# Kernel optimization log

Hardware: AMD Instinct MI355X
Metric: run time of the kernel (lower is better)

## Reference

```python
import jax, jax.numpy as jnp
import numpy as np

N = 50000       # nodes
E = 1600000     # edges (before self-loops)
H = 4           # heads
C = 32          # channels per head
G = 64          # graphs in batch
NEG_SLOPE = 0.2


def gat_conv(x, src, dst, W, att_src, att_dst, bias):
    # x: [N, Fin]; W: [Fin, H*C]; att_*: [H, C]; bias: [H*C]
    h = (x @ W).reshape(N, H, C)                       # [N, H, C]
    a_src = jnp.einsum('nhc,hc->nh', h, att_src)       # [N, H]
    a_dst = jnp.einsum('nhc,hc->nh', h, att_dst)       # [N, H]
    e = a_src[src] + a_dst[dst]                        # [E', H]
    e = jax.nn.leaky_relu(e, NEG_SLOPE)
    # softmax over incoming edges of each destination node
    m = jax.ops.segment_max(e, dst, num_segments=N)    # [N, H]
    ex = jnp.exp(e - m[dst])
    denom = jax.ops.segment_sum(ex, dst, num_segments=N)  # [N, H]
    alpha = ex / (denom[dst] + 1e-16)                  # [E', H]
    msg = h[src] * alpha[:, :, None]                   # [E', H, C]
    out = jax.ops.segment_sum(msg, dst, num_segments=N)  # [N, H, C]
    return out.reshape(N, H * C) + bias


def setup_inputs() -> dict:
    key = jax.random.key(0)
    ks = jax.random.split(key, 12)
    x = jax.random.normal(ks[0], (N, 128), dtype=jnp.float32)
    edge_index = jax.random.randint(ks[1], (2, E), 0, N, dtype=jnp.int64)
    batch = jnp.sort(jax.random.randint(ks[2], (N,), 0, G, dtype=jnp.int64))
    s = 0.05
    return {
        'x': x,
        'edge_index': edge_index,
        'batch': batch,
        'W1': jax.random.normal(ks[3], (128, H * C), dtype=jnp.float32) * s,
        'att_src1': jax.random.normal(ks[4], (H, C), dtype=jnp.float32) * s,
        'att_dst1': jax.random.normal(ks[5], (H, C), dtype=jnp.float32) * s,
        'b1': jnp.zeros((H * C,), dtype=jnp.float32),
        'W2': jax.random.normal(ks[6], (H * C, H * C), dtype=jnp.float32) * s,
        'att_src2': jax.random.normal(ks[7], (H, C), dtype=jnp.float32) * s,
        'att_dst2': jax.random.normal(ks[8], (H, C), dtype=jnp.float32) * s,
        'b2': jnp.zeros((H * C,), dtype=jnp.float32),
        'fc_W': jax.random.normal(ks[9], (H * C, 8), dtype=jnp.float32) * s,
        'fc_b': jnp.zeros((8,), dtype=jnp.float32),
    }


def reference(x, edge_index, batch, W1, att_src1, att_dst1, b1,
              W2, att_src2, att_dst2, b2, fc_W, fc_b):
    # add self loops (PyG GATConv default)
    ar = jnp.arange(N, dtype=edge_index.dtype)
    src = jnp.concatenate([edge_index[0], ar])
    dst = jnp.concatenate([edge_index[1], ar])
    h = gat_conv(x, src, dst, W1, att_src1, att_dst1, b1)
    h = jax.nn.elu(h)
    h = gat_conv(h, src, dst, W2, att_src2, att_dst2, b2)
    # global mean pool over graphs
    sums = jax.ops.segment_sum(h, batch, num_segments=G)          # [G, HC]
    cnt = jax.ops.segment_sum(jnp.ones((N,), h.dtype), batch, num_segments=G)
    pooled = sums / jnp.maximum(cnt, 1.0)[:, None]
    logits = pooled @ fc_W + fc_b                                  # [G, 8]
    return jax.nn.log_softmax(logits, axis=1)
```

## Files before the change

### kernel.cpp

```cpp
#include <hip/hip_runtime.h>
#include <math.h>

#define HC 128
#define GG 64
#define NEG 0.2f
#define TILE 8192
#define BW 128
#define SLOT 8192
#define LDA 136
#define GBS 32

typedef __attribute__((ext_vector_type(8))) short short8;
typedef __attribute__((ext_vector_type(4))) float floatx4;
typedef __attribute__((ext_vector_type(2))) float floatx2;

static __device__ __forceinline__ float leaky(float x) { return x > 0.f ? x : NEG * x; }

static __device__ __forceinline__ unsigned short f2bf(float f) {
    unsigned u = __float_as_uint(f);
    u += 0x7FFF + ((u >> 16) & 1);
    return (unsigned short)(u >> 16);
}

#if __has_builtin(__builtin_amdgcn_cvt_pk_f32_fp8) && __has_builtin(__builtin_amdgcn_cvt_pk_fp8_f32)
template <bool HI>
static __device__ __forceinline__ floatx2 fp8pair(unsigned int w) {
    return __builtin_amdgcn_cvt_pk_f32_fp8((int)w, HI);
}
static __device__ __forceinline__ unsigned int f32x2_fp8(float a, float b) {
    return ((unsigned int)__builtin_amdgcn_cvt_pk_fp8_f32(a, b, 0, false)) & 0xFFFFu;
}
#else
static __device__ __forceinline__ float fp8one(unsigned v) {
    unsigned e = (v >> 3) & 15u, m = v & 7u;
    float mag = e ? __uint_as_float(((e + 120u) << 23) | (m << 20))
                  : (float)m * 0.001953125f;
    return (v & 0x80u) ? -mag : mag;
}
template <bool HI>
static __device__ __forceinline__ floatx2 fp8pair(unsigned int w) {
    unsigned h = HI ? (w >> 16) : w;
    floatx2 r; r.x = fp8one(h & 0xFFu); r.y = fp8one((h >> 8) & 0xFFu);
    return r;
}
static __device__ __forceinline__ unsigned fp8enc(float f) {
    unsigned u = __float_as_uint(f);
    unsigned s = (u >> 24) & 0x80u;
    float a = fabsf(f);
    if (a >= 448.f) return s | 0x7Eu;
    if (a < 0.015625f) {
        unsigned m = (unsigned)(int)rintf(a * 512.f);
        return s | m;
    }
    u = __float_as_uint(a);
    u += 0xFFFFFu + ((u >> 20) & 1u);
    unsigned e8 = (u >> 23) - 120u;
    if (e8 >= 16u) return s | 0x7Eu;
    return s | (e8 << 3) | ((u >> 20) & 7u);
}
static __device__ __forceinline__ unsigned int f32x2_fp8(float a, float b) {
    return fp8enc(a) | (fp8enc(b) << 8);
}
#endif

static __device__ __forceinline__ void acc16(floatx2* acc, float w, const uint4& d) {
    floatx2 w2 = {w, w};
    acc[0] += w2 * fp8pair<false>(d.x);
    acc[1] += w2 * fp8pair<true>(d.x);
    acc[2] += w2 * fp8pair<false>(d.y);
    acc[3] += w2 * fp8pair<true>(d.y);
    acc[4] += w2 * fp8pair<false>(d.z);
    acc[5] += w2 * fp8pair<true>(d.z);
    acc[6] += w2 * fp8pair<false>(d.w);
    acc[7] += w2 * fp8pair<true>(d.w);
}

__global__ __launch_bounds__(256) void setup_k(const float* __restrict__ W1,
                                               const float* __restrict__ W2,
                                               unsigned short* __restrict__ Wt1,
                                               unsigned short* __restrict__ Wt2,
                                               int* __restrict__ gbcur,
                                               const int* __restrict__ batch,
                                               int* __restrict__ node_end,
                                               int* __restrict__ row_start,
                                               int NB, int Nn, int M) {
    int i = blockIdx.x * 256 + threadIdx.x;
    if (i < NB) gbcur[i * GBS] = i * SLOT;
    if (i == 0) row_start[Nn] = M;
    if (i < 32768) {
        const float* W = (i >> 14) ? W2 : W1;
        unsigned short* Wt = (i >> 14) ? Wt2 : Wt1;
        int d = i & 16383;
        int j = d & 7;
        int m = (d >> 3) & 15;
        int qf = d >> 7;
        int q = qf & 3;
        int f = qf >> 2;
        int kb = f & 3;
        int ct = f >> 2;
        int n = ct * 16 + m;
        int k = kb * 32 + q * 8 + j;
        Wt[d] = f2bf(W[k * 128 + n]);
    }
    if (i < Nn) {
        int b = batch[i];
        if (i == 0) {
            for (int g = 0; g < b; g++) node_end[g] = 0;
        }
        int bn = (i + 1 < Nn) ? batch[i + 1] : GG;
        for (int g = b; g < bn; g++) node_end[g] = i + 1;
    }
}

__global__ __launch_bounds__(512) void fused_k(const int* __restrict__ ei,
                                               int* __restrict__ gbcur,
                                               unsigned int* __restrict__ staging,
                                               int E, int M, int NB, int NBIN,
                                               const float* __restrict__ X,
                                               const unsigned short* __restrict__ Wt,
                                               const float* __restrict__ att_s,
                                               const float* __restrict__ att_d,
                                               unsigned char* __restrict__ H8,
                                               float* __restrict__ a_src,
                                               float* __restrict__ a_dst,
                                               int n_rows) {
    __shared__ __align__(16) char smem[39040];
    const int tid = threadIdx.x;

    if ((int)blockIdx.x < NBIN) {
        unsigned int* reorder = (unsigned int*)smem;
        int* s_cnt  = (int*)(smem + 32768);
        int* s_off  = (int*)(smem + 34816);
        int* s_run  = (int*)(smem + 36864);
        int* s_wsum = (int*)(smem + 38912);
        const int lane = tid & 63, wid = tid >> 6;
        const int tbase = blockIdx.x * TILE;
        const int tcnt = min(TILE, M - tbase);
        const bool fullLoad = (tbase + TILE <= E);
        const bool fullTile = (tcnt == TILE);

        unsigned int pk[16];
        if (fullLoad) {
            int s_[16], d_[16];
            #pragma unroll
            for (int q = 0; q < 16; q++) s_[q] = ei[tbase + tid + q * 512];
            #pragma unroll
            for (int q = 0; q < 16; q++) d_[q] = ei[E + tbase + tid + q * 512];
            #pragma unroll
            for (int q = 0; q < 16; q++)
                pk[q] = ((unsigned int)d_[q] << 16) | (unsigned int)s_[q];
        } else {
            #pragma unroll
            for (int q = 0; q < 16; q++) {
                int t = tid + q * 512;
                if (t < tcnt) {
                    int i = tbase + t;
                    int src, dst;
                    if (i < E) { src = ei[i]; dst = ei[E + i]; }
                    else       { src = dst = i - E; }
                    pk[q] = ((unsigned int)dst << 16) | (unsigned int)src;
                }
            }
        }

        for (int i = tid; i < NB; i += 512) s_cnt[i] = 0;
        __syncthreads();

        int rr[16];
        if (fullTile) {
            #pragma unroll
            for (int q = 0; q < 16; q++) rr[q] = atomicAdd(&s_cnt[pk[q] >> 23], 1);
        } else {
            #pragma unroll
            for (int q = 0; q < 16; q++) {
                int t = tid + q * 512;
                if (t < tcnt) rr[q] = atomicAdd(&s_cnt[pk[q] >> 23], 1);
            }
        }
        __syncthreads();

        {
            int v = (tid < NB) ? s_cnt[tid] : 0;
            int incl = v;
            #pragma unroll
            for (int off = 1; off < 64; off <<= 1) {
                int u = __shfl_up(incl, off);
                if (lane >= off) incl += u;
            }
            if (lane == 63) s_wsum[wid] = incl;
            __syncthreads();
            if (tid == 0) {
                int run = 0;
                #pragma unroll
                for (int w = 0; w < 8; w++) { int tv = s_wsum[w]; s_wsum[w] = run; run += tv; }
            }
            __syncthreads();
            int excl = s_wsum[wid] + incl - v;
            if (tid < NB) s_off[tid] = excl;
        }
        __syncthreads();

        for (int b = tid; b < NB; b += 512)
            s_run[b] = atomicAdd(&gbcur[b * GBS], s_cnt[b]);
        if (fullTile) {
            #pragma unroll
            for (int q = 0; q < 16; q++)
                reorder[s_off[pk[q] >> 23] + rr[q]] = pk[q];
        } else {
            #pragma unroll
            for (int q = 0; q < 16; q++) {
                int t = tid + q * 512;
                if (t < tcnt) reorder[s_off[pk[q] >> 23] + rr[q]] = pk[q];
            }
        }
        __syncthreads();

        if (fullTile) {
            unsigned int p[16];
            #pragma unroll
            for (int q = 0; q < 16; q++) p[q] = reorder[tid + q * 512];
            #pragma unroll
            for (int q = 0; q < 16; q++) {
                int t = tid + q * 512;
                int b = p[q] >> 23;
                staging[s_run[b] + (t - s_off[b])] = p[q];
            }
        } else {
            #pragma unroll
            for (int q = 0; q < 16; q++) {
                int t = tid + q * 512;
                if (t < tcnt) {
                    unsigned int p = reorder[t];
                    int b = p >> 23;
                    staging[s_run[b] + (t - s_off[b])] = p;
                }
            }
        }
    } else {
        unsigned short* As = (unsigned short*)smem;
        const int gb = blockIdx.x - NBIN;
        const int row0 = gb * 128;

        for (int i = tid; i < 4096; i += 512) {
            int r = i >> 5;
            int c4 = (i & 31) << 2;
            int gr = row0 + r;
            float4 v = (gr < n_rows) ? ((const float4*)&X[(size_t)gr * 128])[i & 31]
                                     : make_float4(0.f, 0.f, 0.f, 0.f);
            ushort4 bv = {f2bf(v.x), f2bf(v.y), f2bf(v.z), f2bf(v.w)};
            *(ushort4*)&As[r * LDA + c4] = bv;
        }
        __syncthreads();

        const int lane = tid & 63;
        const int wave = tid >> 6;
        const int m = lane & 15;
        const int quad = lane >> 4;
        const int wr = wave * 16;

        floatx4 acc[8];
        #pragma unroll
        for (int ct = 0; ct < 8; ct++) acc[ct] = (floatx4){0.f, 0.f, 0.f, 0.f};

        #pragma unroll
        for (int kb = 0; kb < 4; kb++) {
            short8 x0 = *(const short8*)&As[(wr + m) * LDA + kb * 32 + quad * 8];
            #pragma unroll
            for (int ct = 0; ct < 8; ct++) {
                short8 wf = *(const short8*)&Wt[(((ct * 4 + kb) * 4) + quad) * 128 + m * 8];
                acc[ct] = __builtin_amdgcn_mfma_f32_16x16x32_bf16(wf, x0, acc[ct], 0, 0, 0);
            }
        }

        const int q4 = quad * 4;
        int node = row0 + wr + m;
        bool vld = node < n_rows;
        float ps[4] = {0.f, 0.f, 0.f, 0.f};
        float pd[4] = {0.f, 0.f, 0.f, 0.f};
        #pragma unroll
        for (int ct = 0; ct < 8; ct++) {
            floatx4 v = acc[ct];
            int c0 = ct * 16 + q4;
            float4 avs = *(const float4*)&att_s[c0];
            float4 avd = *(const float4*)&att_d[c0];
            int h = ct >> 1;
            ps[h] += v[0] * avs.x + v[1] * avs.y + v[2] * avs.z + v[3] * avs.w;
            pd[h] += v[0] * avd.x + v[1] * avd.y + v[2] * avd.z + v[3] * avd.w;
            if (vld) {
                unsigned pk01 = f32x2_fp8(v[0], v[1]);
                unsigned pk23 = f32x2_fp8(v[2], v[3]);
                *(unsigned*)&H8[(size_t)node * 128 + c0] = pk01 | (pk23 << 16);
            }
        }
        #pragma unroll
        for (int h = 0; h < 4; h++) {
            ps[h] += __shfl_xor(ps[h], 16); ps[h] += __shfl_xor(ps[h], 32);
            pd[h] += __shfl_xor(pd[h], 16); pd[h] += __shfl_xor(pd[h], 32);
        }
        if (lane < 16 && vld) {
            float4 s4 = {ps[0], ps[1], ps[2], ps[3]};
            float4 d4 = {pd[0], pd[1], pd[2], pd[3]};
            *(float4*)&a_src[node * 4] = s4;
            *(float4*)&a_dst[node * 4] = d4;
        }
    }
}

__global__ __launch_bounds__(512) void unbin_k(const unsigned int* __restrict__ staging,
                                               const int* __restrict__ gbcur,
                                               int* __restrict__ row_start,
                                               unsigned short* __restrict__ srcs, int Nn) {
    __shared__ int s_cnt[BW];
    __shared__ int s_cur[BW];
    __shared__ int s_w[8];
    int b = blockIdx.x, t = threadIdx.x;
    int sbase = b * SLOT;
    int cnt = gbcur[b * GBS] - sbase;

    int pacc = 0;
    for (int i = t; i < b; i += 512) pacc += gbcur[i * GBS] - i * SLOT;
    #pragma unroll
    for (int off = 1; off < 64; off <<= 1) pacc += __shfl_xor(pacc, off);
    if ((t & 63) == 0) s_w[t >> 6] = pacc;
    __syncthreads();
    int bb = 0;
    #pragma unroll
    for (int w = 0; w < 8; w++) bb += s_w[w];
    __syncthreads();

    int n0 = b * BW;
    if (t < BW) s_cnt[t] = 0;
    __syncthreads();

    unsigned int pk[16];
    int rr[16];
    #pragma unroll
    for (int q = 0; q < 16; q++) {
        int j = t + q * 512;
        if (j < cnt) pk[q] = staging[sbase + j];
    }
    #pragma unroll
    for (int q = 0; q < 16; q++) {
        int j = t + q * 512;
        if (j < cnt) rr[q] = atomicAdd(&s_cnt[(pk[q] >> 16) & (BW - 1)], 1);
    }
    __syncthreads();

    int v = (t < BW) ? s_cnt[t] : 0;
    int incl = v;
    #pragma unroll
    for (int off = 1; off < 64; off <<= 1) {
        int u = __shfl_up(incl, off);
        if ((t & 63) >= off) incl += u;
    }
    if (t < BW && (t & 63) == 63) s_w[t >> 6] = incl;
    __syncthreads();
    int excl = incl - v + ((t >= 64 && t < BW) ? s_w[0] : 0);
    if (t < BW) {
        s_cur[t] = bb + excl;
        if (n0 + t < Nn) row_start[n0 + t] = bb + excl;
    }
    __syncthreads();

    #pragma unroll
    for (int q = 0; q < 16; q++) {
        int j = t + q * 512;
        if (j < cnt)
            srcs[s_cur[(pk[q] >> 16) & (BW - 1)] + rr[q]] = (unsigned short)(pk[q] & 0xFFFFu);
    }
}

__global__ __launch_bounds__(512) void agg_gemm2_k(const unsigned char* __restrict__ H8,
                                                   const float* __restrict__ a_src,
                                                   const float* __restrict__ a_dst,
                                                   const int* __restrict__ row_start,
                                                   const unsigned short* __restrict__ srcs,
                                                   const float* __restrict__ bias,
                                                   const unsigned short* __restrict__ Wt,
                                                   const float* __restrict__ att_s,
                                                   const float* __restrict__ att_d,
                                                   unsigned char* __restrict__ H8b,
                                                   float* __restrict__ a_src2,
                                                   float* __restrict__ a_dst2,
                                                   int n_rows) {
    __shared__ unsigned short As[64 * LDA];
    const int tid = threadIdx.x;
    const int row0 = blockIdx.x * 64;

    {
        int r = tid >> 3;
        int n = row0 + r;
        int li = tid & 7;
        int hd = li >> 1;
        bool vld = n < n_rows;

        float o[16];
        #pragma unroll
        for (int k = 0; k < 16; k++) o[k] = 0.f;

        if (vld) {
            int base = row_start[n];
            int end = row_start[n + 1];
            float adh = a_dst[n * 4 + hd];

            floatx2 acc[8];
            #pragma unroll
            for (int k = 0; k < 8; k++) acc[k] = (floatx2){0.f, 0.f};
            float wsum = 0.f;

            int j = base;
            int head_n = min(end - j, (4 - (base & 3)) & 3);
            for (int q = 0; q < head_n; q++, j++) {
                int s0 = srcs[j];
                float w0 = __expf(leaky(a_src[s0 * 4 + hd] + adh));
                uint4 d0 = *(const uint4*)&H8[(size_t)s0 * 128 + li * 16];
                acc16(acc, w0, d0);
                wsum += w0;
            }
            for (; j + 4 <= end; j += 4) {
                uint2 sv = *(const uint2*)&srcs[j];
                int s0 = sv.x & 0xFFFFu, s1 = sv.x >> 16;
                int s2 = sv.y & 0xFFFFu, s3 = sv.y >> 16;
                float a0 = a_src[s0 * 4 + hd];
                float a1 = a_src[s1 * 4 + hd];
                float a2 = a_src[s2 * 4 + hd];
                float a3 = a_src[s3 * 4 + hd];
                uint4 d0 = *(const uint4*)&H8[(size_t)s0 * 128 + li * 16];
                uint4 d1 = *(const uint4*)&H8[(size_t)s1 * 128 + li * 16];
                uint4 d2 = *(const uint4*)&H8[(size_t)s2 * 128 + li * 16];
                uint4 d3 = *(const uint4*)&H8[(size_t)s3 * 128 + li * 16];
                float w0 = __expf(leaky(a0 + adh));
                float w1 = __expf(leaky(a1 + adh));
                float w2 = __expf(leaky(a2 + adh));
                float w3 = __expf(leaky(a3 + adh));
                acc16(acc, w0, d0);
                acc16(acc, w1, d1);
                acc16(acc, w2, d2);
                acc16(acc, w3, d3);
                wsum += (w0 + w1) + (w2 + w3);
            }
            for (; j < end; j++) {
                int s0 = srcs[j];
                float w0 = __expf(leaky(a_src[s0 * 4 + hd] + adh));
                uint4 d0 = *(const uint4*)&H8[(size_t)s0 * 128 + li * 16];
                acc16(acc, w0, d0);
                wsum += w0;
            }

            float ih = 1.0f / (wsum + 1e-16f);
            #pragma unroll
            for (int k = 0; k < 8; k++) {
                float2 bv = *(const float2*)&bias[li * 16 + 2 * k];
                o[2 * k]     = acc[k].x * ih + bv.x;
                o[2 * k + 1] = acc[k].y * ih + bv.y;
            }
            #pragma unroll
            for (int k = 0; k < 16; k++) o[k] = o[k] > 0.f ? o[k] : __expf(o[k]) - 1.f;
        }

        unsigned int pk2[8];
        #pragma unroll
        for (int k = 0; k < 8; k++)
            pk2[k] = ((unsigned)f2bf(o[2 * k + 1]) << 16) | (unsigned)f2bf(o[2 * k]);
        unsigned short* Ap = &As[r * LDA + li * 16];
        *(uint4*)Ap       = make_uint4(pk2[0], pk2[1], pk2[2], pk2[3]);
        *(uint4*)(Ap + 8) = make_uint4(pk2[4], pk2[5], pk2[6], pk2[7]);
    }
    __syncthreads();

    {
        const int lane = tid & 63;
        const int wave = tid >> 6;
        const int m = lane & 15;
        const int quad = lane >> 4;
        const int wr = (wave & 3) * 16;
        const int ctb = (wave >> 2) * 4;

        floatx4 acc[4];
        #pragma unroll
        for (int c = 0; c < 4; c++) acc[c] = (floatx4){0.f, 0.f, 0.f, 0.f};

        #pragma unroll
        for (int kb = 0; kb < 4; kb++) {
            short8 x0 = *(const short8*)&As[(wr + m) * LDA + kb * 32 + quad * 8];
            #pragma unroll
            for (int c = 0; c < 4; c++) {
                int ct = ctb + c;
                short8 wf = *(const short8*)&Wt[(((ct * 4 + kb) * 4) + quad) * 128 + m * 8];
                acc[c] = __builtin_amdgcn_mfma_f32_16x16x32_bf16(wf, x0, acc[c], 0, 0, 0);
            }
        }

        const int q4 = quad * 4;
        int node = row0 + wr + m;
        bool vld = node < n_rows;
        float ps[2] = {0.f, 0.f};
        float pd[2] = {0.f, 0.f};
        #pragma unroll
        for (int c = 0; c < 4; c++) {
            floatx4 v = acc[c];
            int ct = ctb + c;
            int c0 = ct * 16 + q4;
            float4 avs = *(const float4*)&att_s[c0];
            float4 avd = *(const float4*)&att_d[c0];
            int h = c >> 1;
            ps[h] += v[0] * avs.x + v[1] * avs.y + v[2] * avs.z + v[3] * avs.w;
            pd[h] += v[0] * avd.x + v[1] * avd.y + v[2] * avd.z + v[3] * avd.w;
            if (vld) {
                unsigned pk01 = f32x2_fp8(v[0], v[1]);
                unsigned pk23 = f32x2_fp8(v[2], v[3]);
                *(unsigned*)&H8b[(size_t)node * 128 + c0] = pk01 | (pk23 << 16);
            }
        }
        #pragma unroll
        for (int h = 0; h < 2; h++) {
            ps[h] += __shfl_xor(ps[h], 16); ps[h] += __shfl_xor(ps[h], 32);
            pd[h] += __shfl_xor(pd[h], 16); pd[h] += __shfl_xor(pd[h], 32);
        }
        if (lane < 16 && vld) {
            float2 s2 = {ps[0], ps[1]};
            float2 d2 = {pd[0], pd[1]};
            *(float2*)&a_src2[node * 4 + (ctb >> 1)] = s2;
            *(float2*)&a_dst2[node * 4 + (ctb >> 1)] = d2;
        }
    }
}

__global__ __launch_bounds__(256) void gat_agg2(const unsigned char* __restrict__ H8,
                                                const float* __restrict__ a_src,
                                                const float* __restrict__ a_dst,
                                                const int* __restrict__ row_start,
                                                const unsigned short* __restrict__ srcs,
                                                const float* __restrict__ bias,
                                                const int* __restrict__ batch,
                                                float* __restrict__ partial,
                                                int n_rows) {
    __shared__ float ls[32][128];
    __shared__ int sg[32];
    int n = (blockIdx.x * 256 + threadIdx.x) >> 3;
    int li = threadIdx.x & 7;
    int hd = li >> 1;
    bool vld = n < n_rows;

    float o[16];
    #pragma unroll
    for (int k = 0; k < 16; k++) o[k] = 0.f;

    if (vld) {
        int base = row_start[n];
        int end = row_start[n + 1];
        float adh = a_dst[n * 4 + hd];

        floatx2 acc[8];
        #pragma unroll
        for (int k = 0; k < 8; k++) acc[k] = (floatx2){0.f, 0.f};
        float wsum = 0.f;

        int j = base;
        int head_n = min(end - j, (4 - (base & 3)) & 3);
        for (int q = 0; q < head_n; q++, j++) {
            int s0 = srcs[j];
            float w0 = __expf(leaky(a_src[s0 * 4 + hd] + adh));
            uint4 d0 = *(const uint4*)&H8[(size_t)s0 * 128 + li * 16];
            acc16(acc, w0, d0);
            wsum += w0;
        }
        for (; j + 4 <= end; j += 4) {
            uint2 sv = *(const uint2*)&srcs[j];
            int s0 = sv.x & 0xFFFFu, s1 = sv.x >> 16;
            int s2 = sv.y & 0xFFFFu, s3 = sv.y >> 16;
            float a0 = a_src[s0 * 4 + hd];
            float a1 = a_src[s1 * 4 + hd];
            float a2 = a_src[s2 * 4 + hd];
            float a3 = a_src[s3 * 4 + hd];
            uint4 d0 = *(const uint4*)&H8[(size_t)s0 * 128 + li * 16];
            uint4 d1 = *(const uint4*)&H8[(size_t)s1 * 128 + li * 16];
            uint4 d2 = *(const uint4*)&H8[(size_t)s2 * 128 + li * 16];
            uint4 d3 = *(const uint4*)&H8[(size_t)s3 * 128 + li * 16];
            float w0 = __expf(leaky(a0 + adh));
            float w1 = __expf(leaky(a1 + adh));
            float w2 = __expf(leaky(a2 + adh));
            float w3 = __expf(leaky(a3 + adh));
            acc16(acc, w0, d0);
            acc16(acc, w1, d1);
            acc16(acc, w2, d2);
            acc16(acc, w3, d3);
            wsum += (w0 + w1) + (w2 + w3);
        }
        for (; j < end; j++) {
            int s0 = srcs[j];
            float w0 = __expf(leaky(a_src[s0 * 4 + hd] + adh));
            uint4 d0 = *(const uint4*)&H8[(size_t)s0 * 128 + li * 16];
            acc16(acc, w0, d0);
            wsum += w0;
        }

        float ih = 1.0f / (wsum + 1e-16f);
        #pragma unroll
        for (int k = 0; k < 8; k++) {
            float2 bv = *(const float2*)&bias[li * 16 + 2 * k];
            o[2 * k]     = acc[k].x * ih + bv.x;
            o[2 * k + 1] = acc[k].y * ih + bv.y;
        }
    }

    int nl = threadIdx.x >> 3;
    int n0b = blockIdx.x * 32;
    float* row = &ls[nl][li * 16];
    *(float4*)&row[0]  = (float4){o[0], o[1], o[2], o[3]};
    *(float4*)&row[4]  = (float4){o[4], o[5], o[6], o[7]};
    *(float4*)&row[8]  = (float4){o[8], o[9], o[10], o[11]};
    *(float4*)&row[12] = (float4){o[12], o[13], o[14], o[15]};
    if (li == 0) sg[nl] = vld ? min(batch[n] - batch[n0b], 3) : 0;
    __syncthreads();
    int t = threadIdx.x;
    if (t < 128) {
        float a0 = 0.f, a1 = 0.f, a2 = 0.f, a3 = 0.f;
        #pragma unroll 8
        for (int r = 0; r < 32; r++) {
            float v = ls[r][t];
            int gr = sg[r];
            a0 += (gr == 0) ? v : 0.f;
            a1 += (gr == 1) ? v : 0.f;
            a2 += (gr == 2) ? v : 0.f;
            a3 += (gr == 3) ? v : 0.f;
        }
        float* pp = &partial[(size_t)blockIdx.x * 4 * 128];
        pp[t] = a0;
        pp[128 + t] = a1;
        pp[256 + t] = a2;
        pp[384 + t] = a3;
    }
}

__global__ __launch_bounds__(64) void head_k(const float* __restrict__ partial,
                                             const int* __restrict__ node_end,
                                             const int* __restrict__ batch,
                                             const float* __restrict__ fcW,
                                             const float* __restrict__ fcb,
                                             float* __restrict__ out, int n_rows) {
    __shared__ float p[128];
    __shared__ float lg[8];
    int g = blockIdx.x, t = threadIdx.x;
    int s = (g > 0) ? node_end[g - 1] : 0;
    int e = node_end[g];
    float cnt = fmaxf((float)(e - s), 1.0f);
    float v0 = 0.f, v1 = 0.f;
    if (e > s) {
        int b0 = s >> 5;
        int b1 = (e - 1) >> 5;
        for (int b = b0; b <= b1; b++) {
            int slot = g - batch[b * 32];
            if (slot < 0 || slot > 3) continue;
            const float* pp = &partial[((size_t)b * 4 + slot) * 128];
            v0 += pp[t];
            v1 += pp[64 + t];
        }
    }
    p[t] = v0 / cnt;
    p[t + 64] = v1 / cnt;
    __syncthreads();
    if (t < 8) {
        float sacc = fcb[t];
        for (int k = 0; k < 128; k++) sacc += p[k] * fcW[k * 8 + t];
        lg[t] = sacc;
    }
    __syncthreads();
    if (t == 0) {
        float m = lg[0];
        for (int j = 1; j < 8; j++) m = fmaxf(m, lg[j]);
        float se = 0.f;
        for (int j = 0; j < 8; j++) se += expf(lg[j] - m);
        float lse = logf(se) + m;
        for (int j = 0; j < 8; j++) out[g * 8 + j] = lg[j] - lse;
    }
}

extern "C" void kernel_launch(void* const* d_in, const int* in_sizes, int n_in,
                              void* d_out, int out_size, void* d_ws, size_t ws_size,
                              hipStream_t stream) {
    const float* x    = (const float*)d_in[0];
    const int*   ei   = (const int*)d_in[1];
    const int*   batch= (const int*)d_in[2];
    const float* W1   = (const float*)d_in[3];
    const float* as1  = (const float*)d_in[4];
    const float* ad1  = (const float*)d_in[5];
    const float* b1   = (const float*)d_in[6];
    const float* W2   = (const float*)d_in[7];
    const float* as2  = (const float*)d_in[8];
    const float* ad2  = (const float*)d_in[9];
    const float* b2   = (const float*)d_in[10];
    const float* fcW  = (const float*)d_in[11];
    const float* fcb  = (const float*)d_in[12];
    float* out = (float*)d_out;

    const int Nn = in_sizes[0] / HC;
    const int E  = in_sizes[1] / 2;
    const int M  = E + Nn;
    const int NB = (Nn + BW - 1) / BW;
    const int NBIN = (M + TILE - 1) / TILE;
    const int GB1 = (Nn + 127) / 128;
    const int AGB = (Nn + 63) / 64;
    const int NBLK2 = (Nn + 31) / 32;

    char* ws = (char*)d_ws;
    size_t off = 0;
    auto alloc = [&](size_t bytes) -> char* {
        char* p = ws + off;
        off = (off + bytes + 255) & ~(size_t)255;
        return p;
    };
    unsigned int* staging = (unsigned int*)alloc((size_t)NB * SLOT * 4);
    unsigned char* H8  = (unsigned char*)alloc((size_t)Nn * HC);
    unsigned char* H8b = (unsigned char*)alloc((size_t)Nn * HC);
    float* asrc      = (float*)alloc((size_t)Nn * 4 * 4);
    float* adst      = (float*)alloc((size_t)Nn * 4 * 4);
    float* asrc2     = (float*)alloc((size_t)Nn * 4 * 4);
    float* adst2     = (float*)alloc((size_t)Nn * 4 * 4);
    unsigned short* srcs = (unsigned short*)alloc((size_t)M * 2);
    int*   row_start = (int*)alloc((size_t)(Nn + 1) * 4);
    float* partial   = (float*)alloc((size_t)NBLK2 * 4 * HC * 4);
    int*   node_end  = (int*)alloc((size_t)GG * 4);
    int*   gbcur     = (int*)alloc((size_t)NB * GBS * 4);
    unsigned short* Wt1 = (unsigned short*)alloc(16384 * 2);
    unsigned short* Wt2 = (unsigned short*)alloc(16384 * 2);

    setup_k<<<(Nn + 255) / 256, 256, 0, stream>>>(W1, W2, Wt1, Wt2, gbcur, batch,
                                                  node_end, row_start, NB, Nn, M);
    fused_k<<<NBIN + GB1, 512, 0, stream>>>(ei, gbcur, staging, E, M, NB, NBIN,
                                            x, Wt1, as1, ad1, H8, asrc, adst, Nn);
    unbin_k<<<NB, 512, 0, stream>>>(staging, gbcur, row_start, srcs, Nn);
    agg_gemm2_k<<<AGB, 512, 0, stream>>>(H8, asrc, adst, row_start, srcs, b1,
                                         Wt2, as2, ad2, H8b, asrc2, adst2, Nn);
    gat_agg2<<<NBLK2, 256, 0, stream>>>(H8b, asrc2, adst2, row_start, srcs, b2,
                                        batch, partial, Nn);
    head_k<<<GG, 64, 0, stream>>>(partial, node_end, batch, fcW, fcb, out, Nn);
}
```

Before: 230.1 us.

## Split each node's edge list across two thread groups in aggregation kernels

Both GAT aggregation kernels now give each destination node 16 threads instead of 8. Each group of 8 walks half of the node's incoming edges, and the partial sums are combined with a cross-lane shuffle. Block sizes double to 1024 and 512 threads. In the fused GEMM stage each of the 16 waves now computes two column tiles instead of four. The aim is more memory-level parallelism for the gather-bound edge loops, at the cost of extra shuffles, a second head/tail loop per half, and half the threads sitting idle during the shared-memory writes.

```diff
diff --git a/kernel.cpp b/kernel.cpp
--- a/kernel.cpp
+++ b/kernel.cpp
@@ -73,6 +73,51 @@
     acc[5] += w2 * fp8pair<true>(d.z);
     acc[6] += w2 * fp8pair<false>(d.w);
     acc[7] += w2 * fp8pair<true>(d.w);
+}
+
+static __device__ __forceinline__ void agg_range(const unsigned char* __restrict__ H8,
+                                                 const float* __restrict__ a_src,
+                                                 const unsigned short* __restrict__ srcs,
+                                                 int jb, int je, int li, int hd, float adh,
+                                                 floatx2* acc, float& wsum) {
+    int j = jb;
+    int head_n = min(je - j, (4 - (jb & 3)) & 3);
+    for (int q = 0; q < head_n; q++, j++) {
+        int s0 = srcs[j];
+        float w0 = __expf(leaky(a_src[s0 * 4 + hd] + adh));
+        uint4 d0 = *(const uint4*)&H8[(size_t)s0 * 128 + li * 16];
+        acc16(acc, w0, d0);
+        wsum += w0;
+    }
+    for (; j + 4 <= je; j += 4) {
+        uint2 sv = *(const uint2*)&srcs[j];
+        int s0 = sv.x & 0xFFFFu, s1 = sv.x >> 16;
+        int s2 = sv.y & 0xFFFFu, s3 = sv.y >> 16;
+        float a0 = a_src[s0 * 4 + hd];
+        float a1 = a_src[s1 * 4 + hd];
+        float a2 = a_src[s2 * 4 + hd];
+        float a3 = a_src[s3 * 4 + hd];
+        uint4 d0 = *(const uint4*)&H8[(size_t)s0 * 128 + li * 16];
+        uint4 d1 = *(const uint4*)&H8[(size_t)s1 * 128 + li * 16];
+        uint4 d2 = *(const uint4*)&H8[(size_t)s2 * 128 + li * 16];
+        uint4 d3 = *(const uint4*)&H8[(size_t)s3 * 128 + li * 16];
+        float w0 = __expf(leaky(a0 + adh));
+        float w1 = __expf(leaky(a1 + adh));
+        float w2 = __expf(leaky(a2 + adh));
+        float w3 = __expf(leaky(a3 + adh));
+        acc16(acc, w0, d0);
+        acc16(acc, w1, d1);
+        acc16(acc, w2, d2);
+        acc16(acc, w3, d3);
+        wsum += (w0 + w1) + (w2 + w3);
+    }
+    for (; j < je; j++) {
+        int s0 = srcs[j];
+        float w0 = __expf(leaky(a_src[s0 * 4 + hd] + adh));
+        uint4 d0 = *(const uint4*)&H8[(size_t)s0 * 128 + li * 16];
+        acc16(acc, w0, d0);
+        wsum += w0;
+    }
 }
 
 __global__ __launch_bounds__(256) void setup_k(const float* __restrict__ W1,
@@ -370,27 +415,28 @@
     }
 }
 
-__global__ __launch_bounds__(512) void agg_gemm2_k(const unsigned char* __restrict__ H8,
-                                                   const float* __restrict__ a_src,
-                                                   const float* __restrict__ a_dst,
-                                                   const int* __restrict__ row_start,
-                                                   const unsigned short* __restrict__ srcs,
-                                                   const float* __restrict__ bias,
-                                                   const unsigned short* __restrict__ Wt,
-                                                   const float* __restrict__ att_s,
-                                                   const float* __restrict__ att_d,
-                                                   unsigned char* __restrict__ H8b,
-                                                   float* __restrict__ a_src2,
-                                                   float* __restrict__ a_dst2,
-                                                   int n_rows) {
+__global__ __launch_bounds__(1024) void agg_gemm2_k(const unsigned char* __restrict__ H8,
+                                                    const float* __restrict__ a_src,
+                                                    const float* __restrict__ a_dst,
+                                                    const int* __restrict__ row_start,
+                                                    const unsigned short* __restrict__ srcs,
+                                                    const float* __restrict__ bias,
+                                                    const unsigned short* __restrict__ Wt,
+                                                    const float* __restrict__ att_s,
+                                                    const float* __restrict__ att_d,
+                                                    unsigned char* __restrict__ H8b,
+                                                    float* __restrict__ a_src2,
+                                                    float* __restrict__ a_dst2,
+                                                    int n_rows) {
     __shared__ unsigned short As[64 * LDA];
     const int tid = threadIdx.x;
     const int row0 = blockIdx.x * 64;
 
     {
-        int r = tid >> 3;
+        int r = tid >> 4;
         int n = row0 + r;
         int li = tid & 7;
+        int g = (tid >> 3) & 1;
         int hd = li >> 1;
         bool vld = n < n_rows;
 
@@ -401,6 +447,9 @@
         if (vld) {
             int base = row_start[n];
             int end = row_start[n + 1];
+            int mid = base + ((end - base) >> 1);
+            int jb = g ? mid : base;
+            int je = g ? end : mid;
             float adh = a_dst[n * 4 + hd];
 
             floatx2 acc[8];
@@ -408,44 +457,14 @@
             for (int k = 0; k < 8; k++) acc[k] = (floatx2){0.f, 0.f};
             float wsum = 0.f;
 
-            int j = base;
-            int head_n = min(end - j, (4 - (base & 3)) & 3);
-            for (int q = 0; q < head_n; q++, j++) {
-                int s0 = srcs[j];
-                float w0 = __expf(leaky(a_src[s0 * 4 + hd] + adh));
-                uint4 d0 = *(const uint4*)&H8[(size_t)s0 * 128 + li * 16];
-                acc16(acc, w0, d0);
-                wsum += w0;
-            }
-            for (; j + 4 <= end; j += 4) {
-                uint2 sv = *(const uint2*)&srcs[j];
-                int s0 = sv.x & 0xFFFFu, s1 = sv.x >> 16;
-                int s2 = sv.y & 0xFFFFu, s3 = sv.y >> 16;
-                float a0 = a_src[s0 * 4 + hd];
-                float a1 = a_src[s1 * 4 + hd];
-                float a2 = a_src[s2 * 4 + hd];
-                float a3 = a_src[s3 * 4 + hd];
-                uint4 d0 = *(const uint4*)&H8[(size_t)s0 * 128 + li * 16];
-                uint4 d1 = *(const uint4*)&H8[(size_t)s1 * 128 + li * 16];
-                uint4 d2 = *(const uint4*)&H8[(size_t)s2 * 128 + li * 16];
-                uint4 d3 = *(const uint4*)&H8[(size_t)s3 * 128 + li * 16];
-                float w0 = __expf(leaky(a0 + adh));
-                float w1 = __expf(leaky(a1 + adh));
-                float w2 = __expf(leaky(a2 + adh));
-                float w3 = __expf(leaky(a3 + adh));
-                acc16(acc, w0, d0);
-                acc16(acc, w1, d1);
-                acc16(acc, w2, d2);
-                acc16(acc, w3, d3);
-                wsum += (w0 + w1) + (w2 + w3);
-            }
-            for (; j < end; j++) {
-                int s0 = srcs[j];
-                float w0 = __expf(leaky(a_src[s0 * 4 + hd] + adh));
-                uint4 d0 = *(const uint4*)&H8[(size_t)s0 * 128 + li * 16];
-                acc16(acc, w0, d0);
-                wsum += w0;
-            }
+            agg_range(H8, a_src, srcs, jb, je, li, hd, adh, acc, wsum);
+
+            #pragma unroll
+            for (int k = 0; k < 8; k++) {
+                acc[k].x += __shfl_xor(acc[k].x, 8);
+                acc[k].y += __shfl_xor(acc[k].y, 8);
+            }
+            wsum += __shfl_xor(wsum, 8);
 
             float ih = 1.0f / (wsum + 1e-16f);
             #pragma unroll
@@ -458,13 +477,15 @@
             for (int k = 0; k < 16; k++) o[k] = o[k] > 0.f ? o[k] : __expf(o[k]) - 1.f;
         }
 
-        unsigned int pk2[8];
-        #pragma unroll
-        for (int k = 0; k < 8; k++)
-            pk2[k] = ((unsigned)f2bf(o[2 * k + 1]) << 16) | (unsigned)f2bf(o[2 * k]);
-        unsigned short* Ap = &As[r * LDA + li * 16];
-        *(uint4*)Ap       = make_uint4(pk2[0], pk2[1], pk2[2], pk2[3]);
-        *(uint4*)(Ap + 8) = make_uint4(pk2[4], pk2[5], pk2[6], pk2[7]);
+        if (g == 0) {
+            unsigned int pk2[8];
+            #pragma unroll
+            for (int k = 0; k < 8; k++)
+                pk2[k] = ((unsigned)f2bf(o[2 * k + 1]) << 16) | (unsigned)f2bf(o[2 * k]);
+            unsigned short* Ap = &As[r * LDA + li * 16];
+            *(uint4*)Ap       = make_uint4(pk2[0], pk2[1], pk2[2], pk2[3]);
+            *(uint4*)(Ap + 8) = make_uint4(pk2[4], pk2[5], pk2[6], pk2[7]);
+        }
     }
     __syncthreads();
 
@@ -474,17 +495,17 @@
         const int m = lane & 15;
         const int quad = lane >> 4;
         const int wr = (wave & 3) * 16;
-        const int ctb = (wave >> 2) * 4;
-
-        floatx4 acc[4];
-        #pragma unroll
-        for (int c = 0; c < 4; c++) acc[c] = (floatx4){0.f, 0.f, 0.f, 0.f};
+        const int ctb = (wave >> 2) * 2;
+
+        floatx4 acc[2];
+        #pragma unroll
+        for (int c = 0; c < 2; c++) acc[c] = (floatx4){0.f, 0.f, 0.f, 0.f};
 
         #pragma unroll
         for (int kb = 0; kb < 4; kb++) {
             short8 x0 = *(const short8*)&As[(wr + m) * LDA + kb * 32 + quad * 8];
             #pragma unroll
-            for (int c = 0; c < 4; c++) {
+            for (int c = 0; c < 2; c++) {
                 int ct = ctb + c;
                 short8 wf = *(const short8*)&Wt[(((ct * 4 + kb) * 4) + quad) * 128 + m * 8];
                 acc[c] = __builtin_amdgcn_mfma_f32_16x16x32_bf16(wf, x0, acc[c], 0, 0, 0);
@@ -494,39 +515,33 @@
         const int q4 = quad * 4;
         int node = row0 + wr + m;
         bool vld = node < n_rows;
-        float ps[2] = {0.f, 0.f};
-        float pd[2] = {0.f, 0.f};
-        #pragma unroll
-        for (int c = 0; c < 4; c++) {
+        float ps = 0.f, pd = 0.f;
+        #pragma unroll
+        for (int c = 0; c < 2; c++) {
             floatx4 v = acc[c];
             int ct = ctb + c;
             int c0 = ct * 16 + q4;
             float4 avs = *(const float4*)&att_s[c0];
             float4 avd = *(const float4*)&att_d[c0];
-            int h = c >> 1;
-            ps[h] += v[0] * avs.x + v[1] * avs.y + v[2] * avs.z + v[3] * avs.w;
-            pd[h] += v[0] * avd.x + v[1] * avd.y + v[2] * avd.z + v[3] * avd.w;
+            ps += v[0] * avs.x + v[1] * avs.y + v[2] * avs.z + v[3] * avs.w;
+            pd += v[0] * avd.x + v[1] * avd.y + v[2] * avd.z + v[3] * avd.w;
             if (vld) {
                 unsigned pk01 = f32x2_fp8(v[0], v[1]);
                 unsigned pk23 = f32x2_fp8(v[2], v[3]);
                 *(unsigned*)&H8b[(size_t)node * 128 + c0] = pk01 | (pk23 << 16);
             }
         }
-        #pragma unroll
-        for (int h = 0; h < 2; h++) {
-            ps[h] += __shfl_xor(ps[h], 16); ps[h] += __shfl_xor(ps[h], 32);
-            pd[h] += __shfl_xor(pd[h], 16); pd[h] += __shfl_xor(pd[h], 32);
-        }
+        ps += __shfl_xor(ps, 16); ps += __shfl_xor(ps, 32);
+        pd += __shfl_xor(pd, 16); pd += __shfl_xor(pd, 32);
         if (lane < 16 && vld) {
-            float2 s2 = {ps[0], ps[1]};
-            float2 d2 = {pd[0], pd[1]};
-            *(float2*)&a_src2[node * 4 + (ctb >> 1)] = s2;
-            *(float2*)&a_dst2[node * 4 + (ctb >> 1)] = d2;
-        }
-    }
-}
-
-__global__ __launch_bounds__(256) void gat_agg2(const unsigned char* __restrict__ H8,
+            int h = ctb >> 1;
+            a_src2[node * 4 + h] = ps;
+            a_dst2[node * 4 + h] = pd;
+        }
+    }
+}
+
+__global__ __launch_bounds__(512) void gat_agg2(const unsigned char* __restrict__ H8,
                                                 const float* __restrict__ a_src,
                                                 const float* __restrict__ a_dst,
                                                 const int* __restrict__ row_start,
@@ -537,8 +552,10 @@
                                                 int n_rows) {
     __shared__ float ls[32][128];
     __shared__ int sg[32];
-    int n = (blockIdx.x * 256 + threadIdx.x) >> 3;
+    int nl = threadIdx.x >> 4;
+    int n = blockIdx.x * 32 + nl;
     int li = threadIdx.x & 7;
+    int g = (threadIdx.x >> 3) & 1;
     int hd = li >> 1;
     bool vld = n < n_rows;
 
@@ -549,6 +566,9 @@
     if (vld) {
         int base = row_start[n];
         int end = row_start[n + 1];
+        int mid = base + ((end - base) >> 1);
+        int jb = g ? mid : base;
+        int je = g ? end : mid;
         float adh = a_dst[n * 4 + hd];
 
         floatx2 acc[8];
@@ -556,44 +576,14 @@
         for (int k = 0; k < 8; k++) acc[k] = (floatx2){0.f, 0.f};
         float wsum = 0.f;
 
-        int j = base;
-        int head_n = min(end - j, (4 - (base & 3)) & 3);
-        for (int q = 0; q < head_n; q++, j++) {
-            int s0 = srcs[j];
-            float w0 = __expf(leaky(a_src[s0 * 4 + hd] + adh));
-            uint4 d0 = *(const uint4*)&H8[(size_t)s0 * 128 + li * 16];
-            acc16(acc, w0, d0);
-            wsum += w0;
-        }
-        for (; j + 4 <= end; j += 4) {
-            uint2 sv = *(const uint2*)&srcs[j];
-            int s0 = sv.x & 0xFFFFu, s1 = sv.x >> 16;
-            int s2 = sv.y & 0xFFFFu, s3 = sv.y >> 16;
-            float a0 = a_src[s0 * 4 + hd];
-            float a1 = a_src[s1 * 4 + hd];
-            float a2 = a_src[s2 * 4 + hd];
-            float a3 = a_src[s3 * 4 + hd];
-            uint4 d0 = *(const uint4*)&H8[(size_t)s0 * 128 + li * 16];
-            uint4 d1 = *(const uint4*)&H8[(size_t)s1 * 128 + li * 16];
-            uint4 d2 = *(const uint4*)&H8[(size_t)s2 * 128 + li * 16];
-            uint4 d3 = *(const uint4*)&H8[(size_t)s3 * 128 + li * 16];
-            float w0 = __expf(leaky(a0 + adh));
-            float w1 = __expf(leaky(a1 + adh));
-            float w2 = __expf(leaky(a2 + adh));
-            float w3 = __expf(leaky(a3 + adh));
-            acc16(acc, w0, d0);
-            acc16(acc, w1, d1);
-            acc16(acc, w2, d2);
-            acc16(acc, w3, d3);
-            wsum += (w0 + w1) + (w2 + w3);
-        }
-        for (; j < end; j++) {
-            int s0 = srcs[j];
-            float w0 = __expf(leaky(a_src[s0 * 4 + hd] + adh));
-            uint4 d0 = *(const uint4*)&H8[(size_t)s0 * 128 + li * 16];
-            acc16(acc, w0, d0);
-            wsum += w0;
-        }
+        agg_range(H8, a_src, srcs, jb, je, li, hd, adh, acc, wsum);
+
+        #pragma unroll
+        for (int k = 0; k < 8; k++) {
+            acc[k].x += __shfl_xor(acc[k].x, 8);
+            acc[k].y += __shfl_xor(acc[k].y, 8);
+        }
+        wsum += __shfl_xor(wsum, 8);
 
         float ih = 1.0f / (wsum + 1e-16f);
         #pragma unroll
@@ -604,14 +594,15 @@
         }
     }
 
-    int nl = threadIdx.x >> 3;
     int n0b = blockIdx.x * 32;
-    float* row = &ls[nl][li * 16];
-    *(float4*)&row[0]  = (float4){o[0], o[1], o[2], o[3]};
-    *(float4*)&row[4]  = (float4){o[4], o[5], o[6], o[7]};
-    *(float4*)&row[8]  = (float4){o[8], o[9], o[10], o[11]};
-    *(float4*)&row[12] = (float4){o[12], o[13], o[14], o[15]};
-    if (li == 0) sg[nl] = vld ? min(batch[n] - batch[n0b], 3) : 0;
+    if (g == 0) {
+        float* row = &ls[nl][li * 16];
+        *(float4*)&row[0]  = (float4){o[0], o[1], o[2], o[3]};
+        *(float4*)&row[4]  = (float4){o[4], o[5], o[6], o[7]};
+        *(float4*)&row[8]  = (float4){o[8], o[9], o[10], o[11]};
+        *(float4*)&row[12] = (float4){o[12], o[13], o[14], o[15]};
+        if (li == 0) sg[nl] = vld ? min(batch[n] - batch[n0b], 3) : 0;
+    }
     __syncthreads();
     int t = threadIdx.x;
     if (t < 128) {
@@ -730,9 +721,9 @@
     fused_k<<<NBIN + GB1, 512, 0, stream>>>(ei, gbcur, staging, E, M, NB, NBIN,
                                             x, Wt1, as1, ad1, H8, asrc, adst, Nn);
     unbin_k<<<NB, 512, 0, stream>>>(staging, gbcur, row_start, srcs, Nn);
-    agg_gemm2_k<<<AGB, 512, 0, stream>>>(H8, asrc, adst, row_start, srcs, b1,
-                                         Wt2, as2, ad2, H8b, asrc2, adst2, Nn);
-    gat_agg2<<<NBLK2, 256, 0, stream>>>(H8b, asrc2, adst2, row_start, srcs, b2,
+    agg_gemm2_k<<<AGB, 1024, 0, stream>>>(H8, asrc, adst, row_start, srcs, b1,
+                                          Wt2, as2, ad2, H8b, asrc2, adst2, Nn);
+    gat_agg2<<<NBLK2, 512, 0, stream>>>(H8b, asrc2, adst2, row_start, srcs, b2,
                                         batch, partial, Nn);
     head_k<<<GG, 64, 0, stream>>>(partial, node_end, batch, fcW, fcb, out, Nn);
 }
```

Result: slower. 252.4 us (+9.7%).
